# Optimization experiments

Hardware: AMD Instinct MI355X
Metric: run time of the kernel (lower is better)

The kernel has to match this reference:

```python
import jax, jax.numpy as jnp
import numpy as np

V_TH = 1.0    # firing threshold (init kwarg `thresh`)
ALPHA = 1.0   # surrogate-gradient sharpness (init kwarg `alpha`)

# Heaviside spike with surrogate gradient (ATan surrogate, standard for IF neurons).
@jax.custom_vjp
def spike(m):
    return (m >= V_TH).astype(m.dtype)

def _spike_fwd(m):
    return spike(m), m

def _spike_bwd(m, g):
    sg = ALPHA / (2.0 * (1.0 + (jnp.pi / 2.0 * ALPHA * (m - V_TH)) ** 2))
    return (g * sg,)

spike.defvjp(_spike_fwd, _spike_bwd)

def if_forward(x_seq):
    """Integrate-and-fire over leading time dim: m_t = v_{t-1} + x_t,
    y_t = H(m_t - v_th), v_t = m_t - y_t * v_th (soft reset)."""
    def step(v, x):
        m = v + x                  # integrate
        y = spike(m)               # threshold
        v_new = m - y * V_TH       # soft reset
        return v_new, y
    v0 = jnp.zeros_like(x_seq[0])
    _, y_seq = jax.lax.scan(step, v0, x_seq)
    return y_seq

def setup_inputs() -> dict:
    key = jax.random.key(0)
    T, B, N = 32, 16, 65536  # [time, batch, neurons]
    x = jax.random.normal(key, (T, B, N), dtype=jnp.float32)
    return {"x": x}

def reference(x):
    return if_forward(x)
```

## Files before the change

kernel.cpp:

```cpp
#include <hip/hip_runtime.h>


#define T_STEPS 32

__global__ __launch_bounds__(256) void if_fwd_kernel(const float4* __restrict__ x,
                                                     float4* __restrict__ y,
                                                     int bn4) {
    const int i = blockIdx.x * blockDim.x + threadIdx.x;
    if (i >= bn4) return;

    float4 v = make_float4(0.f, 0.f, 0.f, 0.f);

#pragma unroll
    for (int t = 0; t < T_STEPS; ++t) {
        const size_t off = (size_t)t * (size_t)bn4 + (size_t)i;
        float4 xt = x[off];

        float4 m;
        m.x = v.x + xt.x;
        m.y = v.y + xt.y;
        m.z = v.z + xt.z;
        m.w = v.w + xt.w;

        float4 s;
        s.x = (m.x >= 1.0f) ? 1.0f : 0.0f;
        s.y = (m.y >= 1.0f) ? 1.0f : 0.0f;
        s.z = (m.z >= 1.0f) ? 1.0f : 0.0f;
        s.w = (m.w >= 1.0f) ? 1.0f : 0.0f;

        v.x = m.x - s.x;
        v.y = m.y - s.y;
        v.z = m.z - s.z;
        v.w = m.w - s.w;

        y[off] = s;
    }
}

extern "C" void kernel_launch(void* const* d_in, const int* in_sizes, int n_in,
                              void* d_out, int out_size, void* d_ws, size_t ws_size,
                              hipStream_t stream) {
    const float* x = (const float*)d_in[0];
    float* y = (float*)d_out;

    const int total = in_sizes[0];
    const int bn = total / T_STEPS;
    const int bn4 = bn / 4;

    const int block = 256;
    const int grid = (bn4 + block - 1) / block;

    if_fwd_kernel<<<grid, block, 0, stream>>>((const float4*)x, (float4*)y, bn4);
}
```

Measured before the change: 269.7 us.

## Use float2 per thread with register prefetch and nontemporal loads/stores

Halves the per-thread vector width to double the number of threads, prefetches the next four time steps of input into registers, and uses nontemporal loads and stores. It targets low memory-level parallelism and cache pollution in a streaming kernel that is bound by latency. The trade-off is narrower memory transactions per thread and more registers spent on the prefetch buffer.

```diff
diff --git a/kernel.cpp b/kernel.cpp
--- a/kernel.cpp
+++ b/kernel.cpp
@@ -2,38 +2,42 @@
 
 
 #define T_STEPS 32
+#define PF 4
 
-__global__ __launch_bounds__(256) void if_fwd_kernel(const float4* __restrict__ x,
-                                                     float4* __restrict__ y,
-                                                     int bn4) {
+typedef float f32x2 __attribute__((ext_vector_type(2)));
+
+__global__ __launch_bounds__(256) void if_fwd_kernel(const f32x2* __restrict__ x,
+                                                     f32x2* __restrict__ y,
+                                                     int bn2) {
     const int i = blockIdx.x * blockDim.x + threadIdx.x;
-    if (i >= bn4) return;
+    if (i >= bn2) return;
 
-    float4 v = make_float4(0.f, 0.f, 0.f, 0.f);
+    f32x2 buf[PF];
+#pragma unroll
+    for (int t = 0; t < PF; ++t)
+        buf[t] = __builtin_nontemporal_load(&x[(size_t)t * (size_t)bn2 + (size_t)i]);
+
+    float vx = 0.f, vy = 0.f;
 
 #pragma unroll
     for (int t = 0; t < T_STEPS; ++t) {
-        const size_t off = (size_t)t * (size_t)bn4 + (size_t)i;
-        float4 xt = x[off];
+        f32x2 xt = buf[t % PF];
 
-        float4 m;
-        m.x = v.x + xt.x;
-        m.y = v.y + xt.y;
-        m.z = v.z + xt.z;
-        m.w = v.w + xt.w;
+        if (t + PF < T_STEPS)
+            buf[(t + PF) % PF] =
+                __builtin_nontemporal_load(&x[(size_t)(t + PF) * (size_t)bn2 + (size_t)i]);
 
-        float4 s;
-        s.x = (m.x >= 1.0f) ? 1.0f : 0.0f;
-        s.y = (m.y >= 1.0f) ? 1.0f : 0.0f;
-        s.z = (m.z >= 1.0f) ? 1.0f : 0.0f;
-        s.w = (m.w >= 1.0f) ? 1.0f : 0.0f;
+        float mx = vx + xt.x;
+        float my = vy + xt.y;
+        float sx = (mx >= 1.0f) ? 1.0f : 0.0f;
+        float sy = (my >= 1.0f) ? 1.0f : 0.0f;
+        vx = mx - sx;
+        vy = my - sy;
 
-        v.x = m.x - s.x;
-        v.y = m.y - s.y;
-        v.z = m.z - s.z;
-        v.w = m.w - s.w;
-
-        y[off] = s;
+        f32x2 s;
+        s.x = sx;
+        s.y = sy;
+        __builtin_nontemporal_store(s, &y[(size_t)t * (size_t)bn2 + (size_t)i]);
     }
 }
 
@@ -45,10 +49,10 @@
 
     const int total = in_sizes[0];
     const int bn = total / T_STEPS;
-    const int bn4 = bn / 4;
+    const int bn2 = bn / 2;
 
     const int block = 256;
-    const int grid = (bn4 + block - 1) / block;
+    const int grid = (bn2 + block - 1) / block;
 
-    if_fwd_kernel<<<grid, block, 0, stream>>>((const float4*)x, (float4*)y, bn4);
+    if_fwd_kernel<<<grid, block, 0, stream>>>((const f32x2*)x, (f32x2*)y, bn2);
 }
```

Measured after the change: 223.8 us. 17.0% less time.
